# Optimization experiments

Hardware: AMD Instinct MI355X
Metric: run time of the kernel (lower is better)

Reference implementation:

```python
import jax, jax.numpy as jnp
import numpy as np

B, T, H = 64, 1024, 256

def _lstm_cell(x, h, c, Wih, Whh, bih, bhh):
    # torch gate order: i, f, g, o
    gates = x @ Wih.T + h @ Whh.T + bih + bhh  # [B, 4H]
    i, f, g, o = jnp.split(gates, 4, axis=-1)
    i = jax.nn.sigmoid(i)
    f = jax.nn.sigmoid(f)
    g = jnp.tanh(g)
    o = jax.nn.sigmoid(o)
    c_new = f * c + i * g
    h_new = o * jnp.tanh(c_new)
    return h_new, c_new


def setup_inputs() -> dict:
    key = jax.random.key(0)
    ks = jax.random.split(key, 11)
    s = 1.0 / np.sqrt(H)
    def u(k, shape):
        return jax.random.uniform(k, shape, jnp.float32, -s, s)
    return {
        "x": jax.random.normal(ks[0], (B, T, 1), jnp.float32),
        "enc_Wih": u(ks[1], (4 * H, 1)),
        "enc_Whh": u(ks[2], (4 * H, H)),
        "enc_bih": u(ks[3], (4 * H,)),
        "enc_bhh": u(ks[4], (4 * H,)),
        "dec_Wih": u(ks[5], (4 * H, 1)),
        "dec_Whh": u(ks[6], (4 * H, H)),
        "dec_bih": u(ks[7], (4 * H,)),
        "dec_bhh": u(ks[8], (4 * H,)),
        "lin_W": u(ks[9], (1, 2 * H)),
        "lin_b": u(ks[10], (1,)),
    }


def reference(x, enc_Wih, enc_Whh, enc_bih, enc_bhh,
              dec_Wih, dec_Whh, dec_bih, dec_bhh, lin_W, lin_b):
    b = x.shape[0]
    h = x.shape[2] * 0  # placeholder, not used
    hidden = enc_Whh.shape[1]

    x_t = jnp.transpose(x, (1, 0, 2))  # [T, B, 1]

    # ---- encoder: single-layer LSTM over time ----
    def enc_step(carry, xt):
        hh, cc = carry
        hh, cc = _lstm_cell(xt, hh, cc, enc_Wih, enc_Whh, enc_bih, enc_bhh)
        return (hh, cc), hh
    h0 = jnp.zeros((b, hidden), x.dtype)
    (h_last, _), enc_seq = jax.lax.scan(enc_step, (h0, h0), x_t)
    encoder_states = jnp.transpose(enc_seq, (1, 0, 2))  # [B, T, H]

    # ---- decoder: LSTMCell + dot attention + linear, per step ----
    def dec_step(carry, xt):
        hx, cx = carry
        hx, cx = _lstm_cell(xt, hx, cx, dec_Wih, dec_Whh, dec_bih, dec_bhh)
        scores = jnp.einsum('bth,bh->bt', encoder_states, hx)  # dot attention
        attn = jax.nn.softmax(scores, axis=1)
        ctx = jnp.einsum('bt,bth->bh', attn, encoder_states)
        updated = jnp.concatenate([ctx, hx], axis=1)  # [B, 2H]
        res = updated @ lin_W.T + lin_b  # [B, 1]
        return (hx, cx), res

    cx0 = jnp.zeros_like(h_last)
    _, outs = jax.lax.scan(dec_step, (h_last, cx0), x_t)  # [T, B, 1]
    return jnp.transpose(outs, (1, 0, 2))  # [B, T, 1]
```

## Files before the change

kernel.cpp:

```cpp
#include <hip/hip_runtime.h>
#include <math.h>

#define HD 256
#define GD 1024
#define TT 1024
#define BB 64
#define NT 512

__device__ __forceinline__ float sig_(float x)  { return 1.f / (1.f + __expf(-x)); }
__device__ __forceinline__ float tanh_(float x) { return 1.f - 2.f / (1.f + __expf(2.f * x)); }

__global__ __launch_bounds__(256) void prep_kernel(
    const float* __restrict__ eW, const float* __restrict__ eb1, const float* __restrict__ eb2,
    const float* __restrict__ dW, const float* __restrict__ db1, const float* __restrict__ db2,
    float* __restrict__ WTe, float* __restrict__ WTd,
    float* __restrict__ be, float* __restrict__ bd,
    unsigned long long* __restrict__ ex_all)
{
    int idx = blockIdx.x * 256 + threadIdx.x;
    if (idx < GD * HD) {
        int j = idx / HD, k = idx % HD;
        WTe[k * GD + j] = eW[idx];
        WTd[k * GD + j] = dW[idx];
    }
    if (idx < GD) {
        be[idx] = eb1[idx] + eb2[idx];
        bd[idx] = db1[idx] + db2[idx];
    }
    if (idx < 2 * BB * 2 * 256) ex_all[idx] = 0ULL;
}

__global__ __launch_bounds__(NT, 2) void lstm_scan_coop(
    const float* __restrict__ x,
    const float* __restrict__ Wih,
    const float* __restrict__ bias,
    const float* __restrict__ WT,
    const float* __restrict__ h_init,
    float* __restrict__ states,
    unsigned long long* __restrict__ ex)
{
    const int b   = blockIdx.x & 63;
    const int q   = blockIdx.x >> 6;
    const int tid = threadIdx.x;
    const int s   = tid & 3;
    const int jj  = tid >> 2;
    const int gate = jj >> 5;
    const int kk0  = (jj & 31) * 2;
    const int r0   = gate * 64 + kk0;
    const int jg0  = gate * 256 + q * 64 + kk0;

    __shared__ float h_rep[4][264];
    __shared__ float act_s[256];
    __shared__ float x_s[TT];

    float4 w0[16], w1[16];
    {
        const float* basek = WT + (size_t)(s * 64) * GD;
        #pragma unroll
        for (int i = 0; i < 16; ++i) {
            const float* p0 = basek + (size_t)(4 * i) * GD + jg0;
            w0[i] = make_float4(p0[0], p0[GD], p0[2 * GD], p0[3 * GD]);
            const float* p1 = p0 + 1;
            w1[i] = make_float4(p1[0], p1[GD], p1[2 * GD], p1[3 * GD]);
        }
    }
    const float wih0 = Wih[jg0], wih1 = Wih[jg0 + 1];
    const float bj0  = bias[jg0], bj1  = bias[jg0 + 1];

    for (int i = tid; i < TT; i += NT) x_s[i] = x[b * TT + i];
    if (tid < 256) {
        float hv = h_init ? h_init[((size_t)b * TT + (TT - 1)) * HD + tid] : 0.f;
        h_rep[tid >> 6][tid & 63] = hv;
    }
    float c = 0.f;
    __syncthreads();

    for (int t = 0; t < TT; ++t) {
        const float xt = x_s[t];
        float a0p, a1p, a0q = 0.f, a1q = 0.f;
        if (s == 0) { a0p = fmaf(xt, wih0, bj0); a1p = fmaf(xt, wih1, bj1); }
        else        { a0p = 0.f;                 a1p = 0.f; }
        const float4* h4 = (const float4*)(&h_rep[s][0]);
        #pragma unroll
        for (int i = 0; i < 8; ++i) {
            float4 hv = h4[i];
            a0p = fmaf(hv.x, w0[i].x, a0p); a0p = fmaf(hv.y, w0[i].y, a0p);
            a0p = fmaf(hv.z, w0[i].z, a0p); a0p = fmaf(hv.w, w0[i].w, a0p);
            a1p = fmaf(hv.x, w1[i].x, a1p); a1p = fmaf(hv.y, w1[i].y, a1p);
            a1p = fmaf(hv.z, w1[i].z, a1p); a1p = fmaf(hv.w, w1[i].w, a1p);
        }
        #pragma unroll
        for (int i = 8; i < 16; ++i) {
            float4 hv = h4[i];
            a0q = fmaf(hv.x, w0[i].x, a0q); a0q = fmaf(hv.y, w0[i].y, a0q);
            a0q = fmaf(hv.z, w0[i].z, a0q); a0q = fmaf(hv.w, w0[i].w, a0q);
            a1q = fmaf(hv.x, w1[i].x, a1q); a1q = fmaf(hv.y, w1[i].y, a1q);
            a1q = fmaf(hv.z, w1[i].z, a1q); a1q = fmaf(hv.w, w1[i].w, a1q);
        }
        float a0 = a0p + a0q;
        float a1 = a1p + a1q;
        a0 += __shfl_xor(a0, 1); a0 += __shfl_xor(a0, 2);
        a1 += __shfl_xor(a1, 1); a1 += __shfl_xor(a1, 2);
        if (s == 0) {
            float2 av;
            av.x = (gate == 2) ? tanh_(a0) : sig_(a0);
            av.y = (gate == 2) ? tanh_(a1) : sig_(a1);
            *(float2*)(&act_s[r0]) = av;
        }
        __syncthreads();

        unsigned long long* slot = ex + ((size_t)b * 2 + (t & 1)) * 256;
        if (tid < 256) {
            const int dq = tid >> 6, dk = tid & 63;
            if (dq == q) {
                float gi = act_s[dk], gf = act_s[64 + dk], gg = act_s[128 + dk], go = act_s[192 + dk];
                c = fmaf(gf, c, gi * gg);
                float h = go * tanh_(c);
                unsigned long long pk = ((unsigned long long)(unsigned)(t + 1) << 32)
                                      | (unsigned long long)__float_as_uint(h);
                __hip_atomic_store(&slot[tid], pk, __ATOMIC_RELAXED, __HIP_MEMORY_SCOPE_AGENT);
                h_rep[q][dk] = h;
                states[((size_t)(b * TT + t)) * HD + tid] = h;
            } else {
                unsigned long long u;
                do {
                    u = __hip_atomic_load(&slot[tid], __ATOMIC_RELAXED, __HIP_MEMORY_SCOPE_AGENT);
                } while ((unsigned)(u >> 32) != (unsigned)(t + 1));
                h_rep[dq][dk] = __uint_as_float((unsigned)u);
            }
        }
        __syncthreads();
    }
}

__global__ __launch_bounds__(256) void proj_kernel(
    const float* __restrict__ enc_states, const float* __restrict__ dec_hs,
    const float* __restrict__ linW, float* __restrict__ ew, float* __restrict__ hw)
{
    const int lane = threadIdx.x & 63;
    const int wid  = blockIdx.x * 4 + (threadIdx.x >> 6);
    const int nw   = gridDim.x * 4;
    const float4 w1 = ((const float4*)linW)[lane];
    const float4 w2 = ((const float4*)(linW + HD))[lane];
    for (int o = wid; o < BB * TT; o += nw) {
        float4 v1 = ((const float4*)(enc_states + (size_t)o * HD))[lane];
        float4 v2 = ((const float4*)(dec_hs     + (size_t)o * HD))[lane];
        float s1 = v1.x * w1.x + v1.y * w1.y + v1.z * w1.z + v1.w * w1.w;
        float s2 = v2.x * w2.x + v2.y * w2.y + v2.z * w2.z + v2.w * w2.w;
        #pragma unroll
        for (int m = 1; m < 64; m <<= 1) {
            s1 += __shfl_xor(s1, m);
            s2 += __shfl_xor(s2, m);
        }
        if (lane == 0) { ew[o] = s1; hw[o] = s2; }
    }
}

#define TD2  32
#define TEC2 256
#define KC2  32
__global__ __launch_bounds__(256) void attn_kernel(
    const float* __restrict__ enc_states,
    const float* __restrict__ dec_hs,
    const float* __restrict__ ew, const float* __restrict__ hw,
    const float* __restrict__ lin_b,
    float* __restrict__ out)
{
    const int b   = blockIdx.y;
    const int td0 = blockIdx.x * TD2;
    const int tid = threadIdx.x;
    const int tdt = tid >> 5;
    const int tet = tid & 31;

    __shared__ float Hx[HD][TD2 + 4];
    __shared__ float E[KC2][TEC2];

    {
        const int td = tid >> 3;
        const int kc = (tid & 7) * 32;
        const float* src = dec_hs + ((size_t)b * TT + td0 + td) * HD + kc;
        #pragma unroll
        for (int qq = 0; qq < 8; ++qq) {
            float4 v = ((const float4*)(src + qq * 4))[0];
            Hx[kc + qq * 4 + 0][td] = v.x;
            Hx[kc + qq * 4 + 1][td] = v.y;
            Hx[kc + qq * 4 + 2][td] = v.z;
            Hx[kc + qq * 4 + 3][td] = v.w;
        }
    }

    float M[4]  = {-1e30f, -1e30f, -1e30f, -1e30f};
    float Nm[4] = {0.f, 0.f, 0.f, 0.f};
    float Dn[4] = {0.f, 0.f, 0.f, 0.f};

    for (int tc = 0; tc < TT / TEC2; ++tc) {
        const int te0 = tc * TEC2;
        float S[4][8] = {{0.f}};
        for (int kc = 0; kc < HD / KC2; ++kc) {
            const int k0 = kc * KC2;
            __syncthreads();
            {
                const float* src = enc_states + ((size_t)b * TT + te0 + tid) * HD + k0;
                #pragma unroll
                for (int qq = 0; qq < 8; ++qq) {
                    float4 v = ((const float4*)(src + qq * 4))[0];
                    E[qq * 4 + 0][tid] = v.x;
                    E[qq * 4 + 1][tid] = v.y;
                    E[qq * 4 + 2][tid] = v.z;
                    E[qq * 4 + 3][tid] = v.w;
                }
            }
            __syncthreads();
            #pragma unroll 4
            for (int k = 0; k < KC2; ++k) {
                const float4 hx4 = *(const float4*)(&Hx[k0 + k][tdt * 4]);
                #pragma unroll
                for (int i = 0; i < 8; ++i) {
                    const float e = E[k][tet + 32 * i];
                    S[0][i] = fmaf(hx4.x, e, S[0][i]);
                    S[1][i] = fmaf(hx4.y, e, S[1][i]);
                    S[2][i] = fmaf(hx4.z, e, S[2][i]);
                    S[3][i] = fmaf(hx4.w, e, S[3][i]);
                }
            }
        }
        float ewv[8];
        #pragma unroll
        for (int i = 0; i < 8; ++i) ewv[i] = ew[(size_t)b * TT + te0 + tet + 32 * i];
        #pragma unroll
        for (int r = 0; r < 4; ++r) {
            float cm = S[r][0];
            #pragma unroll
            for (int i = 1; i < 8; ++i) cm = fmaxf(cm, S[r][i]);
            #pragma unroll
            for (int m = 1; m < 32; m <<= 1) cm = fmaxf(cm, __shfl_xor(cm, m));
            const float newM  = fmaxf(M[r], cm);
            const float scale = __expf(M[r] - newM);
            float nl = 0.f, dl = 0.f;
            #pragma unroll
            for (int i = 0; i < 8; ++i) {
                const float p = __expf(S[r][i] - newM);
                dl += p;
                nl = fmaf(p, ewv[i], nl);
            }
            #pragma unroll
            for (int m = 1; m < 32; m <<= 1) {
                nl += __shfl_xor(nl, m);
                dl += __shfl_xor(dl, m);
            }
            Nm[r] = Nm[r] * scale + nl;
            Dn[r] = Dn[r] * scale + dl;
            M[r]  = newM;
        }
    }

    if (tet == 0) {
        const float lb = lin_b[0];
        #pragma unroll
        for (int r = 0; r < 4; ++r) {
            const int td = td0 + tdt * 4 + r;
            out[(size_t)b * TT + td] = Nm[r] / Dn[r] + hw[(size_t)b * TT + td] + lb;
        }
    }
}

extern "C" void kernel_launch(void* const* d_in, const int* in_sizes, int n_in,
                              void* d_out, int out_size, void* d_ws, size_t ws_size,
                              hipStream_t stream)
{
    const float* x    = (const float*)d_in[0];
    const float* eWih = (const float*)d_in[1];
    const float* eWhh = (const float*)d_in[2];
    const float* ebih = (const float*)d_in[3];
    const float* ebhh = (const float*)d_in[4];
    const float* dWih = (const float*)d_in[5];
    const float* dWhh = (const float*)d_in[6];
    const float* dbih = (const float*)d_in[7];
    const float* dbhh = (const float*)d_in[8];
    const float* linW = (const float*)d_in[9];
    const float* linb = (const float*)d_in[10];
    float* out = (float*)d_out;

    float* p = (float*)d_ws;
    float* WTe = p;        p += (size_t)GD * HD;
    float* WTd = p;        p += (size_t)GD * HD;
    float* be  = p;        p += GD;
    float* bd  = p;        p += GD;
    float* enc_states = p; p += (size_t)BB * TT * HD;
    float* dec_hs = p;     p += (size_t)BB * TT * HD;
    float* ew = p;         p += (size_t)BB * TT;
    float* hw = p;         p += (size_t)BB * TT;
    unsigned long long* ex_e = (unsigned long long*)p; p += (size_t)BB * 2 * 256 * 2;
    unsigned long long* ex_d = (unsigned long long*)p; p += (size_t)BB * 2 * 256 * 2;

    prep_kernel<<<(GD * HD + 255) / 256, 256, 0, stream>>>(
        eWhh, ebih, ebhh, dWhh, dbih, dbhh, WTe, WTd, be, bd, ex_e);

    {
        const float* hi = nullptr;
        void* args[] = {(void*)&x, (void*)&eWih, (void*)&be, (void*)&WTe,
                        (void*)&hi, (void*)&enc_states, (void*)&ex_e};
        hipLaunchCooperativeKernel((void*)lstm_scan_coop, dim3(256), dim3(NT),
                                   args, 0, stream);
    }
    {
        const float* hi = enc_states;
        void* args[] = {(void*)&x, (void*)&dWih, (void*)&bd, (void*)&WTd,
                        (void*)&hi, (void*)&dec_hs, (void*)&ex_d};
        hipLaunchCooperativeKernel((void*)lstm_scan_coop, dim3(256), dim3(NT),
                                   args, 0, stream);
    }

    proj_kernel<<<256, 256, 0, stream>>>(enc_states, dec_hs, linW, ew, hw);
    attn_kernel<<<dim3(TT / TD2, BB), 256, 0, stream>>>(enc_states, dec_hs, ew, hw, linb, out);
}
```

Baseline: 3.943 ms.

## Overlap decoder attention with decoder LSTM scan and fuse projections into scans

Merges the decoder scan and the attention into one kernel. Scan blocks publish per-32-step progress counters, and attention blocks spin on those counters so they can process finished time tiles while the recurrence is still running. The linear-projection dot products are folded into the scans as per-quarter partial sums (qew/qhw), which removes the separate projection kernel. The polling loop now uses pipelined inline-asm loads and s_setprio on the critical path, the exchange buffer is shared via a tag offset, and the attention tiling changes. The design relies on co-residency of scan and attention blocks now that the cooperative launch is gone, which risks deadlock. It also contains a leftover line computing hw_s from qhw that is immediately overwritten.

```diff
diff --git a/kernel.cpp b/kernel.cpp
--- a/kernel.cpp
+++ b/kernel.cpp
@@ -15,7 +15,8 @@
     const float* __restrict__ dW, const float* __restrict__ db1, const float* __restrict__ db2,
     float* __restrict__ WTe, float* __restrict__ WTd,
     float* __restrict__ be, float* __restrict__ bd,
-    unsigned long long* __restrict__ ex_all)
+    unsigned long long* __restrict__ ex,
+    unsigned* __restrict__ prog4)
 {
     int idx = blockIdx.x * 256 + threadIdx.x;
     if (idx < GD * HD) {
@@ -27,20 +28,20 @@
         be[idx] = eb1[idx] + eb2[idx];
         bd[idx] = db1[idx] + db2[idx];
     }
-    if (idx < 2 * BB * 2 * 256) ex_all[idx] = 0ULL;
-}
-
-__global__ __launch_bounds__(NT, 2) void lstm_scan_coop(
-    const float* __restrict__ x,
-    const float* __restrict__ Wih,
-    const float* __restrict__ bias,
-    const float* __restrict__ WT,
-    const float* __restrict__ h_init,
-    float* __restrict__ states,
-    unsigned long long* __restrict__ ex)
-{
-    const int b   = blockIdx.x & 63;
-    const int q   = blockIdx.x >> 6;
+    if (idx < BB * 2 * 256) ex[idx] = 0ULL;
+    if (idx < BB * 4) prog4[idx] = 0u;
+}
+
+__device__ __forceinline__ void scan_body(
+    const float* __restrict__ x, const float* __restrict__ Wih,
+    const float* __restrict__ bias, const float* __restrict__ WT,
+    const float* __restrict__ h_init, float* __restrict__ states,
+    unsigned long long* __restrict__ ex, unsigned tag0,
+    const float* __restrict__ lw, float* __restrict__ qdot,
+    unsigned* __restrict__ prog4,
+    float* x_s, float* h_rep , float* act_s ,
+    int b, int q)
+{
     const int tid = threadIdx.x;
     const int s   = tid & 3;
     const int jj  = tid >> 2;
@@ -49,10 +50,6 @@
     const int r0   = gate * 64 + kk0;
     const int jg0  = gate * 256 + q * 64 + kk0;
 
-    __shared__ float h_rep[4][264];
-    __shared__ float act_s[256];
-    __shared__ float x_s[TT];
-
     float4 w0[16], w1[16];
     {
         const float* basek = WT + (size_t)(s * 64) * GD;
@@ -66,21 +63,25 @@
     }
     const float wih0 = Wih[jg0], wih1 = Wih[jg0 + 1];
     const float bj0  = bias[jg0], bj1  = bias[jg0 + 1];
+    const float lwd  = lw[tid & 255];
 
     for (int i = tid; i < TT; i += NT) x_s[i] = x[b * TT + i];
     if (tid < 256) {
         float hv = h_init ? h_init[((size_t)b * TT + (TT - 1)) * HD + tid] : 0.f;
-        h_rep[tid >> 6][tid & 63] = hv;
+        h_rep[(tid >> 6) * 264 + (tid & 63)] = hv;
     }
     float c = 0.f;
+    int pipe_ok = 1;
     __syncthreads();
 
+    #pragma unroll 1
     for (int t = 0; t < TT; ++t) {
+        __builtin_amdgcn_s_setprio(1);
         const float xt = x_s[t];
         float a0p, a1p, a0q = 0.f, a1q = 0.f;
         if (s == 0) { a0p = fmaf(xt, wih0, bj0); a1p = fmaf(xt, wih1, bj1); }
         else        { a0p = 0.f;                 a1p = 0.f; }
-        const float4* h4 = (const float4*)(&h_rep[s][0]);
+        const float4* h4 = (const float4*)(h_rep + s * 264);
         #pragma unroll
         for (int i = 0; i < 8; ++i) {
             float4 hv = h4[i];
@@ -109,85 +110,162 @@
         }
         __syncthreads();
 
-        unsigned long long* slot = ex + ((size_t)b * 2 + (t & 1)) * 256;
+        const unsigned tag = tag0 + (unsigned)t + 1u;
+        unsigned long long* ssl = ex + ((size_t)b * 2 + (t & 1)) * 256;
         if (tid < 256) {
             const int dq = tid >> 6, dk = tid & 63;
             if (dq == q) {
                 float gi = act_s[dk], gf = act_s[64 + dk], gg = act_s[128 + dk], go = act_s[192 + dk];
                 c = fmaf(gf, c, gi * gg);
                 float h = go * tanh_(c);
-                unsigned long long pk = ((unsigned long long)(unsigned)(t + 1) << 32)
+                unsigned long long pk = ((unsigned long long)tag << 32)
                                       | (unsigned long long)__float_as_uint(h);
-                __hip_atomic_store(&slot[tid], pk, __ATOMIC_RELAXED, __HIP_MEMORY_SCOPE_AGENT);
-                h_rep[q][dk] = h;
+                __hip_atomic_store(&ssl[tid], pk, __ATOMIC_RELAXED, __HIP_MEMORY_SCOPE_AGENT);
+                h_rep[q * 264 + dk] = h;
                 states[((size_t)(b * TT + t)) * HD + tid] = h;
+                __builtin_amdgcn_s_setprio(0);
+                float v = h * lwd;
+                #pragma unroll
+                for (int m = 1; m < 64; m <<= 1) v += __shfl_xor(v, m);
+                if (dk == 0) qdot[((size_t)(b * TT + t)) * 4 + q] = v;
             } else {
-                unsigned long long u;
-                do {
-                    u = __hip_atomic_load(&slot[tid], __ATOMIC_RELAXED, __HIP_MEMORY_SCOPE_AGENT);
-                } while ((unsigned)(u >> 32) != (unsigned)(t + 1));
-                h_rep[dq][dk] = __uint_as_float((unsigned)u);
-            }
+                __builtin_amdgcn_s_setprio(0);
+                unsigned long long u; int got = 0;
+                const unsigned long long* sp = ssl + tid;
+                if (pipe_ok) {
+                    unsigned long long u0, u1;
+                    asm volatile("global_load_dwordx2 %0, %2, off sc0 sc1\n\t"
+                                 "global_load_dwordx2 %1, %2, off sc0 sc1"
+                                 : "=&v"(u0), "=&v"(u1) : "v"(sp));
+                    #pragma unroll 1
+                    for (int it = 0; it < 300; ++it) {
+                        asm volatile("s_waitcnt vmcnt(1)" : "+v"(u0));
+                        if ((unsigned)(u0 >> 32) == tag) { u = u0; got = 1; break; }
+                        asm volatile("global_load_dwordx2 %0, %1, off sc0 sc1"
+                                     : "=&v"(u0) : "v"(sp));
+                        asm volatile("s_waitcnt vmcnt(1)" : "+v"(u1));
+                        if ((unsigned)(u1 >> 32) == tag) { u = u1; got = 1; break; }
+                        asm volatile("global_load_dwordx2 %0, %1, off sc0 sc1"
+                                     : "=&v"(u1) : "v"(sp));
+                    }
+                    asm volatile("s_waitcnt vmcnt(0)" ::: "memory");
+                    if (!got) pipe_ok = 0;
+                }
+                if (!got) {
+                    do {
+                        u = __hip_atomic_load(sp, __ATOMIC_RELAXED, __HIP_MEMORY_SCOPE_AGENT);
+                    } while ((unsigned)(u >> 32) != tag);
+                }
+                h_rep[dq * 264 + dk] = __uint_as_float((unsigned)u);
+            }
+        } else {
+            __builtin_amdgcn_s_setprio(0);
         }
         __syncthreads();
-    }
-}
-
-__global__ __launch_bounds__(256) void proj_kernel(
-    const float* __restrict__ enc_states, const float* __restrict__ dec_hs,
-    const float* __restrict__ linW, float* __restrict__ ew, float* __restrict__ hw)
-{
-    const int lane = threadIdx.x & 63;
-    const int wid  = blockIdx.x * 4 + (threadIdx.x >> 6);
-    const int nw   = gridDim.x * 4;
-    const float4 w1 = ((const float4*)linW)[lane];
-    const float4 w2 = ((const float4*)(linW + HD))[lane];
-    for (int o = wid; o < BB * TT; o += nw) {
-        float4 v1 = ((const float4*)(enc_states + (size_t)o * HD))[lane];
-        float4 v2 = ((const float4*)(dec_hs     + (size_t)o * HD))[lane];
-        float s1 = v1.x * w1.x + v1.y * w1.y + v1.z * w1.z + v1.w * w1.w;
-        float s2 = v2.x * w2.x + v2.y * w2.y + v2.z * w2.z + v2.w * w2.w;
-        #pragma unroll
-        for (int m = 1; m < 64; m <<= 1) {
-            s1 += __shfl_xor(s1, m);
-            s2 += __shfl_xor(s2, m);
-        }
-        if (lane == 0) { ew[o] = s1; hw[o] = s2; }
-    }
-}
-
-#define TD2  32
-#define TEC2 256
-#define KC2  32
-__global__ __launch_bounds__(256) void attn_kernel(
-    const float* __restrict__ enc_states,
-    const float* __restrict__ dec_hs,
-    const float* __restrict__ ew, const float* __restrict__ hw,
-    const float* __restrict__ lin_b,
+        if (prog4 && ((t & 31) == 31) && tid == 0)
+            __hip_atomic_store(&prog4[b * 4 + q], (unsigned)((t + 1) >> 5),
+                               __ATOMIC_RELEASE, __HIP_MEMORY_SCOPE_AGENT);
+    }
+}
+
+__global__ __launch_bounds__(NT, 2) void enc_kernel(
+    const float* __restrict__ x, const float* __restrict__ Wih,
+    const float* __restrict__ bias, const float* __restrict__ WT,
+    float* __restrict__ states, unsigned long long* __restrict__ ex,
+    const float* __restrict__ lw, float* __restrict__ qew)
+{
+    __shared__ float x_s[TT];
+    __shared__ float h_rep[4 * 264];
+    __shared__ float act_s[256];
+    const int b = (int)blockIdx.x & 63;
+    const int q = (int)blockIdx.x >> 6;
+    scan_body(x, Wih, bias, WT, nullptr, states, ex, 0u, lw, qew, nullptr,
+              x_s, h_rep, act_s, b, q);
+}
+
+#define SMEMF 19712
+#define TDA   64
+#define TEC2  256
+#define KC2   8
+__global__ __launch_bounds__(NT, 4) void tail_kernel(
+    const float* __restrict__ x, const float* __restrict__ Wih,
+    const float* __restrict__ bias, const float* __restrict__ WT,
+    const float* __restrict__ enc_states, float* __restrict__ dec_hs,
+    unsigned long long* __restrict__ ex,
+    const float* __restrict__ lw2, float* __restrict__ qhw,
+    unsigned* __restrict__ prog4,
+    const float* __restrict__ qew, const float* __restrict__ lin_b,
     float* __restrict__ out)
 {
-    const int b   = blockIdx.y;
-    const int td0 = blockIdx.x * TD2;
+    __shared__ __align__(16) float smem[SMEMF];
+    const int blk = (int)blockIdx.x;
     const int tid = threadIdx.x;
-    const int tdt = tid >> 5;
-    const int tet = tid & 31;
-
-    __shared__ float Hx[HD][TD2 + 4];
-    __shared__ float E[KC2][TEC2];
+
+    if (blk < 256) {
+        float* x_s   = smem;
+        float* h_rep = smem + 1024;
+        float* act_s = smem + 1024 + 4 * 264;
+        const int b = blk & 63;
+        const int q = blk >> 6;
+        scan_body(x, Wih, bias, WT, enc_states, dec_hs, ex, 1024u, lw2, qhw,
+                  prog4, x_s, h_rep, act_s, b, q);
+        return;
+    }
+
+    const int ai   = blk - 256;
+    const int b    = ai & 63;
+    const int tile = ai >> 6;
+    const int td0  = tile * TDA;
+    float* Hx   = smem;
+    float* E    = smem + 17408;
+    float* hw_s = smem + 17408 + 2048;
+
+    if (tid == 0) {
+        const unsigned need = (unsigned)(tile * 2 + 2);
+        for (;;) {
+            unsigned m0 = __hip_atomic_load(&prog4[b*4+0], __ATOMIC_RELAXED, __HIP_MEMORY_SCOPE_AGENT);
+            unsigned m1 = __hip_atomic_load(&prog4[b*4+1], __ATOMIC_RELAXED, __HIP_MEMORY_SCOPE_AGENT);
+            unsigned m2 = __hip_atomic_load(&prog4[b*4+2], __ATOMIC_RELAXED, __HIP_MEMORY_SCOPE_AGENT);
+            unsigned m3 = __hip_atomic_load(&prog4[b*4+3], __ATOMIC_RELAXED, __HIP_MEMORY_SCOPE_AGENT);
+            unsigned mn = min(min(m0, m1), min(m2, m3));
+            if (mn >= need) break;
+            __builtin_amdgcn_s_sleep(2);
+        }
+        (void)__hip_atomic_load(&prog4[b*4], __ATOMIC_ACQUIRE, __HIP_MEMORY_SCOPE_AGENT);
+    }
+    __syncthreads();
 
     {
         const int td = tid >> 3;
         const int kc = (tid & 7) * 32;
         const float* src = dec_hs + ((size_t)b * TT + td0 + td) * HD + kc;
+        const float4* w2 = (const float4*)(lw2 + kc);
+        float ph = 0.f;
         #pragma unroll
         for (int qq = 0; qq < 8; ++qq) {
             float4 v = ((const float4*)(src + qq * 4))[0];
-            Hx[kc + qq * 4 + 0][td] = v.x;
-            Hx[kc + qq * 4 + 1][td] = v.y;
-            Hx[kc + qq * 4 + 2][td] = v.z;
-            Hx[kc + qq * 4 + 3][td] = v.w;
-        }
-    }
+            float4 w = w2[qq];
+            Hx[(kc + qq * 4 + 0) * 68 + td] = v.x;
+            Hx[(kc + qq * 4 + 1) * 68 + td] = v.y;
+            Hx[(kc + qq * 4 + 2) * 68 + td] = v.z;
+            Hx[(kc + qq * 4 + 3) * 68 + td] = v.w;
+            ph = fmaf(v.x, w.x, ph); ph = fmaf(v.y, w.y, ph);
+            ph = fmaf(v.z, w.z, ph); ph = fmaf(v.w, w.w, ph);
+        }
+        E[td * 8 + (tid & 7)] = ph;
+    }
+    __syncthreads();
+    if (tid < TDA) {
+        float sum = 0.f;
+        #pragma unroll
+        for (int j = 0; j < 8; ++j) sum += E[tid * 8 + j];
+        const float4 h4v = ((const float4*)qhw)[(size_t)b * TT + td0 + tid];
+        hw_s[tid] = sum * 0.f + (h4v.x + h4v.y + h4v.z + h4v.w);
+        hw_s[tid] = sum;
+    }
+
+    const int tdt = tid >> 5;
+    const int tet = tid & 31;
 
     float M[4]  = {-1e30f, -1e30f, -1e30f, -1e30f};
     float Nm[4] = {0.f, 0.f, 0.f, 0.f};
@@ -200,23 +278,21 @@
             const int k0 = kc * KC2;
             __syncthreads();
             {
-                const float* src = enc_states + ((size_t)b * TT + te0 + tid) * HD + k0;
-                #pragma unroll
-                for (int qq = 0; qq < 8; ++qq) {
-                    float4 v = ((const float4*)(src + qq * 4))[0];
-                    E[qq * 4 + 0][tid] = v.x;
-                    E[qq * 4 + 1][tid] = v.y;
-                    E[qq * 4 + 2][tid] = v.z;
-                    E[qq * 4 + 3][tid] = v.w;
-                }
+                const int te = tid & 255, half = tid >> 8;
+                const float* src = enc_states + ((size_t)b * TT + te0 + te) * HD + k0 + half * 4;
+                float4 v = ((const float4*)src)[0];
+                E[(half * 4 + 0) * 256 + te] = v.x;
+                E[(half * 4 + 1) * 256 + te] = v.y;
+                E[(half * 4 + 2) * 256 + te] = v.z;
+                E[(half * 4 + 3) * 256 + te] = v.w;
             }
             __syncthreads();
-            #pragma unroll 4
+            #pragma unroll
             for (int k = 0; k < KC2; ++k) {
-                const float4 hx4 = *(const float4*)(&Hx[k0 + k][tdt * 4]);
+                const float4 hx4 = *(const float4*)(&Hx[(k0 + k) * 68 + tdt * 4]);
                 #pragma unroll
                 for (int i = 0; i < 8; ++i) {
-                    const float e = E[k][tet + 32 * i];
+                    const float e = E[k * 256 + tet + 32 * i];
                     S[0][i] = fmaf(hx4.x, e, S[0][i]);
                     S[1][i] = fmaf(hx4.y, e, S[1][i]);
                     S[2][i] = fmaf(hx4.z, e, S[2][i]);
@@ -226,7 +302,10 @@
         }
         float ewv[8];
         #pragma unroll
-        for (int i = 0; i < 8; ++i) ewv[i] = ew[(size_t)b * TT + te0 + tet + 32 * i];
+        for (int i = 0; i < 8; ++i) {
+            const float4 e4 = ((const float4*)qew)[(size_t)b * TT + te0 + tet + 32 * i];
+            ewv[i] = (e4.x + e4.y) + (e4.z + e4.w);
+        }
         #pragma unroll
         for (int r = 0; r < 4; ++r) {
             float cm = S[r][0];
@@ -258,8 +337,8 @@
         const float lb = lin_b[0];
         #pragma unroll
         for (int r = 0; r < 4; ++r) {
-            const int td = td0 + tdt * 4 + r;
-            out[(size_t)b * TT + td] = Nm[r] / Dn[r] + hw[(size_t)b * TT + td] + lb;
+            const int td = tdt * 4 + r;
+            out[(size_t)b * TT + td0 + td] = Nm[r] / Dn[r] + hw_s[td] + lb;
         }
     }
 }
@@ -288,29 +367,18 @@
     float* bd  = p;        p += GD;
     float* enc_states = p; p += (size_t)BB * TT * HD;
     float* dec_hs = p;     p += (size_t)BB * TT * HD;
-    float* ew = p;         p += (size_t)BB * TT;
-    float* hw = p;         p += (size_t)BB * TT;
-    unsigned long long* ex_e = (unsigned long long*)p; p += (size_t)BB * 2 * 256 * 2;
-    unsigned long long* ex_d = (unsigned long long*)p; p += (size_t)BB * 2 * 256 * 2;
+    float* qew = p;        p += (size_t)BB * TT * 4;
+    float* qhw = p;        p += (size_t)BB * TT * 4;
+    unsigned long long* ex = (unsigned long long*)p; p += (size_t)BB * 2 * 256 * 2;
+    unsigned* prog4 = (unsigned*)p; p += 256;
 
     prep_kernel<<<(GD * HD + 255) / 256, 256, 0, stream>>>(
-        eWhh, ebih, ebhh, dWhh, dbih, dbhh, WTe, WTd, be, bd, ex_e);
-
-    {
-        const float* hi = nullptr;
-        void* args[] = {(void*)&x, (void*)&eWih, (void*)&be, (void*)&WTe,
-                        (void*)&hi, (void*)&enc_states, (void*)&ex_e};
-        hipLaunchCooperativeKernel((void*)lstm_scan_coop, dim3(256), dim3(NT),
-                                   args, 0, stream);
-    }
-    {
-        const float* hi = enc_states;
-        void* args[] = {(void*)&x, (void*)&dWih, (void*)&bd, (void*)&WTd,
-                        (void*)&hi, (void*)&dec_hs, (void*)&ex_d};
-        hipLaunchCooperativeKernel((void*)lstm_scan_coop, dim3(256), dim3(NT),
-                                   args, 0, stream);
-    }
-
-    proj_kernel<<<256, 256, 0, stream>>>(enc_states, dec_hs, linW, ew, hw);
-    attn_kernel<<<dim3(TT / TD2, BB), 256, 0, stream>>>(enc_states, dec_hs, ew, hw, linb, out);
-}
+        eWhh, ebih, ebhh, dWhh, dbih, dbhh, WTe, WTd, be, bd, ex, prog4);
+
+    enc_kernel<<<256, NT, 0, stream>>>(
+        x, eWih, be, WTe, enc_states, ex, linW, qew);
+
+    tail_kernel<<<256 + BB * (TT / TDA), NT, 0, stream>>>(
+        x, dWih, bd, WTd, enc_states, dec_hs, ex, linW + HD, qhw,
+        prog4, qew, linb, out);
+}
```

After: 7.013 ms. 77.9% more time.
